# Kernel tuning notes

Hardware: AMD Instinct MI355X
Metric: run time of the kernel (lower is better)

Reference implementation:

```python
import jax, jax.numpy as jnp
import numpy as np

D_MODEL = 512
N_HEADS = 8
B, S = 2, 2048


def setup_inputs() -> dict:
    key = jax.random.key(0)
    ks = jax.random.split(key, 7)
    scale = 1.0 / np.sqrt(D_MODEL)
    return {
        "q": jax.random.normal(ks[0], (B, S, D_MODEL), jnp.float32),
        "k": jax.random.normal(ks[1], (B, S, D_MODEL), jnp.float32),
        "v": jax.random.normal(ks[2], (B, S, D_MODEL), jnp.float32),
        "Wq_w": jax.random.normal(ks[3], (D_MODEL, D_MODEL), jnp.float32) * scale,
        "Wq_b": jnp.zeros((D_MODEL,), jnp.float32),
        "Wc_w": jax.random.normal(ks[4], (D_MODEL, D_MODEL), jnp.float32) * scale,
        "Wc_b": jnp.zeros((D_MODEL,), jnp.float32),
    }


def _split(x, n_heads):
    b, s, d = x.shape
    return x.reshape(b, s, n_heads, d // n_heads).transpose(0, 2, 1, 3)  # [b,h,s,dh]


def reference(q, k, v, Wq_w, Wq_b, Wc_w, Wc_b):
    # NOTE: original code (faithfully) projects q, k, v all with W_q.
    qp = q @ Wq_w.T + Wq_b
    kp = k @ Wq_w.T + Wq_b
    vp = v @ Wq_w.T + Wq_b
    qh = _split(qp, N_HEADS)  # [b,h,s,dh]
    kh = _split(kp, N_HEADS)
    vh = _split(vp, N_HEADS)
    d_tensor = qh.shape[-1]
    scores = jnp.einsum("bhqd,bhkd->bhqk", qh, kh) / jnp.sqrt(jnp.float32(d_tensor))
    att = jax.nn.softmax(scores, axis=-1)
    out = jnp.einsum("bhqk,bhkd->bhqd", att, vh)
    b, h, s, dh = out.shape
    out = out.transpose(0, 2, 1, 3).reshape(b, s, h * dh)
    return out @ Wc_w.T + Wc_b
```

## Files before the change

### kernel.cpp

```cpp
#include <hip/hip_runtime.h>
#include <hip/hip_bf16.h>
#include <stdint.h>


typedef __bf16 bf16;
typedef __bf16 bvec8 __attribute__((ext_vector_type(8)));
typedef __bf16 bvec4 __attribute__((ext_vector_type(4)));
typedef float  fvec4 __attribute__((ext_vector_type(4)));
typedef float  fvec16 __attribute__((ext_vector_type(16)));
typedef int    ivec4 __attribute__((ext_vector_type(4)));

#define MFMA16(a, b, c) __builtin_amdgcn_mfma_f32_16x16x32_bf16(a, b, c, 0, 0, 0)
#define MFMA32(a, b, c) __builtin_amdgcn_mfma_f32_32x32x16_bf16(a, b, c, 0, 0, 0)

__device__ __forceinline__ void async16(const void* g, void* l) {
  __builtin_amdgcn_global_load_lds(
      (__attribute__((address_space(1))) void*)(g),
      (__attribute__((address_space(3))) void*)(l), 16, 0, 0);
}

__global__ void cvt_all(const float* __restrict__ q, const float* __restrict__ k,
                        const float* __restrict__ v, const float* __restrict__ Wq,
                        const float* __restrict__ Wc, bf16* __restrict__ qkvb,
                        bf16* __restrict__ Wq16, bf16* __restrict__ Wc16) {
  const int t = blockIdx.x * 256 + threadIdx.x;
  const float* src;
  bf16* dst;
  size_t i;
  if (t < 786432) {
    const int which = t >> 18;
    i = (size_t)(t & 262143);
    src = (which == 0) ? q : (which == 1) ? k : v;
    dst = qkvb + ((size_t)which << 21);
  } else if (t < 819200) {
    src = Wq; dst = Wq16; i = (size_t)(t - 786432);
  } else {
    src = Wc; dst = Wc16; i = (size_t)(t - 819200);
  }
  fvec4 a = *(const fvec4*)(src + i * 8);
  fvec4 b = *(const fvec4*)(src + i * 8 + 4);
  bvec8 o;
#pragma unroll
  for (int j = 0; j < 4; ++j) { o[j] = (bf16)a[j]; o[j + 4] = (bf16)b[j]; }
  *(bvec8*)(dst + i * 8) = o;
}

__launch_bounds__(256, 3)
__global__ void proj_gemm(const bf16* __restrict__ X, const bf16* __restrict__ W,
                          const float* __restrict__ bias, bf16* __restrict__ Y,
                          bf16* __restrict__ Yt) {
  __shared__ __attribute__((aligned(16))) char As[2][64 * 128];
  __shared__ __attribute__((aligned(16))) char Bs[2][128 * 128];

  const int tid = threadIdx.x;
  const int w = tid >> 6, l = tid & 63;
  const int wr = w >> 1, wc = w & 1;
  const int l15 = l & 15, lg = l >> 4;
  const int bm0 = blockIdx.x * 64;
  const int bn0 = blockIdx.y * 128;

  fvec4 acc[2][4] = {};

  auto stageA = [&](int buf, int k0) {
#pragma unroll
    for (int j = 0; j < 2; ++j) {
      int c = j * 256 + tid;
      int row = c >> 3, g = (c & 7) ^ (row & 7);
      async16(X + (size_t)(bm0 + row) * 512 + k0 + g * 8, &As[buf][c * 16]);
    }
  };
  auto stageB = [&](int buf, int k0) {
#pragma unroll
    for (int j = 0; j < 4; ++j) {
      int c = j * 256 + tid;
      int row = c >> 3, g = (c & 7) ^ (row & 7);
      async16(W + (size_t)(bn0 + row) * 512 + k0 + g * 8, &Bs[buf][c * 16]);
    }
  };

  stageA(0, 0);
  stageB(0, 0);
  __syncthreads();

  for (int t = 0; t < 8; ++t) {
    const int buf = t & 1;
    if (t < 7) { stageA(buf ^ 1, (t + 1) * 64); stageB(buf ^ 1, (t + 1) * 64); }
#pragma unroll
    for (int kk = 0; kk < 2; ++kk) {
      bvec8 af[2], bfr[4];
      const int g = kk * 4 + lg;
#pragma unroll
      for (int m = 0; m < 2; ++m) {
        int r = wr * 32 + m * 16 + l15;
        af[m] = *(const bvec8*)&As[buf][r * 128 + ((g ^ (r & 7)) << 4)];
      }
#pragma unroll
      for (int n = 0; n < 4; ++n) {
        int r = wc * 64 + n * 16 + l15;
        bfr[n] = *(const bvec8*)&Bs[buf][r * 128 + ((g ^ (r & 7)) << 4)];
      }
#pragma unroll
      for (int m = 0; m < 2; ++m)
#pragma unroll
        for (int n = 0; n < 4; ++n) acc[m][n] = MFMA16(af[m], bfr[n], acc[m][n]);
    }
    __syncthreads();
  }

  const bool trans = (bm0 >= 8192);
  const float scl = (bm0 < 4096) ? 0.18033688011112042f : 1.0f;
#pragma unroll
  for (int n = 0; n < 4; ++n) {
    const int col = bn0 + wc * 64 + n * 16 + l15;
    const float bv = bias[col];
#pragma unroll
    for (int m = 0; m < 2; ++m) {
      const int row0 = bm0 + wr * 32 + m * 16 + lg * 4;
      if (!trans) {
#pragma unroll
        for (int r = 0; r < 4; ++r)
          Y[(size_t)(row0 + r) * 512 + col] = (bf16)((acc[m][n][r] + bv) * scl);
      } else {
        const int m0 = row0 - 8192;
        const int b = m0 >> 11, s = m0 & 2047;
        bvec4 v4;
#pragma unroll
        for (int r = 0; r < 4; ++r) v4[r] = (bf16)(acc[m][n][r] + bv);
        *(bvec4*)&Yt[(size_t)(b * 512 + col) * 2048 + s] = v4;
      }
    }
  }
}

__launch_bounds__(256, 4)
__global__ void attn_kernel(const bf16* __restrict__ qp, const bf16* __restrict__ kp,
                            const bf16* __restrict__ vt, bf16* __restrict__ po01,
                            bf16* __restrict__ po23, float* __restrict__ pl) {
  __shared__ __attribute__((aligned(16))) char Ks[2][64 * 128];
  __shared__ __attribute__((aligned(16))) char Vs[2][64 * 128];

  const int tid = threadIdx.x;
  const int w = tid >> 6, l = tid & 63;
  const int l31 = l & 31, hi = l >> 5;
  const int bh = blockIdx.y, b = bh >> 3, h = bh & 7;
  const int half = blockIdx.z;
  const int kvbase = half * 512;
  const int qw0 = blockIdx.x * 128 + w * 32;

  const bf16* kbase = kp + (size_t)(b * 2048) * 512 + h * 64;
  const bf16* vbase = vt + (size_t)(b * 512 + h * 64) * 2048;

  bvec8 qf[4];
  {
    const bf16* qrow = qp + (size_t)(b * 2048 + qw0 + l31) * 512 + h * 64 + hi * 8;
#pragma unroll
    for (int ks = 0; ks < 4; ++ks) qf[ks] = *(const bvec8*)(qrow + ks * 16);
  }
  bvec8 ones;
#pragma unroll
  for (int e = 0; e < 8; ++e) ones[e] = (bf16)1.0f;

  auto stageK = [&](int buf, int kv0) {
#pragma unroll
    for (int j = 0; j < 2; ++j) {
      int c = j * 256 + tid;
      int row = c >> 3, g = (c & 7) ^ (row & 7);
      async16(kbase + (size_t)(kv0 + row) * 512 + g * 8, &Ks[buf][c * 16]);
    }
  };
  auto stageV = [&](int buf, int kv0) {
#pragma unroll
    for (int j = 0; j < 2; ++j) {
      int c = j * 256 + tid;
      int row = c >> 3, g = (c & 7) ^ (row & 7);
      async16(vbase + (size_t)row * 2048 + kv0 + g * 8, &Vs[buf][c * 16]);
    }
  };

  fvec16 oacc[2] = {};
  fvec16 lacc = {};

  stageK(0, kvbase);
  stageV(0, kvbase);
  __syncthreads();

  for (int t = 0; t < 8; ++t) {
    const int buf = t & 1;
    if (t < 7) {
      stageK(buf ^ 1, kvbase + (t + 1) * 64);
      stageV(buf ^ 1, kvbase + (t + 1) * 64);
    }

    fvec16 sac[2] = {};
    __builtin_amdgcn_s_setprio(1);
#pragma unroll
    for (int ks = 0; ks < 4; ++ks) {
      const int chunk = ks * 2 + hi;
#pragma unroll
      for (int kvb = 0; kvb < 2; ++kvb) {
        const int r = kvb * 32 + l31;
        bvec8 kf = *(const bvec8*)&Ks[buf][r * 128 + ((chunk ^ (r & 7)) << 4)];
        sac[kvb] = MFMA32(kf, qf[ks], sac[kvb]);
      }
    }
    __builtin_amdgcn_s_setprio(0);

    ivec4 pw[4];
#pragma unroll
    for (int f = 0; f < 2; ++f) {
      float p[16];
#pragma unroll
      for (int r2 = 0; r2 < 16; ++r2) p[r2] = exp2f(sac[f][r2]);
      int wv[4][2];
#pragma unroll
      for (int m = 0; m < 4; ++m)
#pragma unroll
        for (int i = 0; i < 2; ++i)
          asm("v_cvt_pk_bf16_f32 %0, %1, %2"
              : "=v"(wv[m][i]) : "v"(p[4 * m + 2 * i]), "v"(p[4 * m + 2 * i + 1]));
#pragma unroll
      for (int i = 0; i < 2; ++i) {
        int a0 = wv[0][i], c0 = wv[1][i];
        asm volatile("v_permlane32_swap_b32 %0, %1" : "+v"(a0), "+v"(c0));
        pw[2 * f][i] = a0; pw[2 * f][2 + i] = c0;
        int a1 = wv[2][i], c1 = wv[3][i];
        asm volatile("v_permlane32_swap_b32 %0, %1" : "+v"(a1), "+v"(c1));
        pw[2 * f + 1][i] = a1; pw[2 * f + 1][2 + i] = c1;
      }
    }

    __builtin_amdgcn_s_setprio(1);
#pragma unroll
    for (int ks = 0; ks < 4; ++ks) {
      const bvec8 pb = __builtin_bit_cast(bvec8, pw[ks]);
      const int chunk = ks * 2 + hi;
#pragma unroll
      for (int dhb = 0; dhb < 2; ++dhb) {
        const int r = dhb * 32 + l31;
        bvec8 vf = *(const bvec8*)&Vs[buf][r * 128 + ((chunk ^ (r & 7)) << 4)];
        oacc[dhb] = MFMA32(pb, vf, oacc[dhb]);
      }
      lacc = MFMA32(pb, ones, lacc);
    }
    __builtin_amdgcn_s_setprio(0);
    __syncthreads();
  }

  bf16* pob = ((half < 2) ? po01 : po23) + (size_t)(half & 1) * 2097152;
#pragma unroll
  for (int dhb = 0; dhb < 2; ++dhb)
#pragma unroll
    for (int r2 = 0; r2 < 16; ++r2) {
      const int q = qw0 + (r2 & 3) + 8 * (r2 >> 2) + 4 * hi;
      pob[(size_t)(b * 2048 + q) * 512 + h * 64 + dhb * 32 + l31] =
          (bf16)oacc[dhb][r2];
    }
  if (l31 == 0) {
#pragma unroll
    for (int r2 = 0; r2 < 16; ++r2) {
      const int q = qw0 + (r2 & 3) + 8 * (r2 >> 2) + 4 * hi;
      pl[half * 32768 + (b * 2048 + q) * 8 + h] = lacc[r2];
    }
  }
}

__global__ void combine_kernel(const bf16* __restrict__ po01, const bf16* __restrict__ po23,
                               const float* __restrict__ pl, bf16* __restrict__ att) {
  const int t = blockIdx.x * 256 + threadIdx.x;
  const int row = t >> 6;
  const int c8 = (t & 63) << 3;
  const int h = c8 >> 6;
  const float inv = 1.0f / (pl[row * 8 + h] + pl[32768 + row * 8 + h] +
                            pl[65536 + row * 8 + h] + pl[98304 + row * 8 + h]);
  bvec8 a0 = *(const bvec8*)(po01 + (size_t)row * 512 + c8);
  bvec8 a1 = *(const bvec8*)(po01 + 2097152 + (size_t)row * 512 + c8);
  bvec8 a2 = *(const bvec8*)(po23 + (size_t)row * 512 + c8);
  bvec8 a3 = *(const bvec8*)(po23 + 2097152 + (size_t)row * 512 + c8);
  bvec8 o;
#pragma unroll
  for (int j = 0; j < 8; ++j)
    o[j] = (bf16)((((float)a0[j] + (float)a1[j]) + ((float)a2[j] + (float)a3[j])) * inv);
  *(bvec8*)(att + (size_t)row * 512 + c8) = o;
}

__launch_bounds__(256, 3)
__global__ void out_gemm(const bf16* __restrict__ X, const bf16* __restrict__ W,
                         const float* __restrict__ bias, float* __restrict__ Y) {
  __shared__ __attribute__((aligned(16))) char As[2][64 * 128];
  __shared__ __attribute__((aligned(16))) char Bs[2][128 * 128];

  const int tid = threadIdx.x;
  const int w = tid >> 6, l = tid & 63;
  const int wr = w >> 1, wc = w & 1;
  const int l15 = l & 15, lg = l >> 4;
  const int bm0 = blockIdx.x * 64;
  const int bn0 = blockIdx.y * 128;

  fvec4 acc[2][4] = {};

  auto stageA = [&](int buf, int k0) {
#pragma unroll
    for (int j = 0; j < 2; ++j) {
      int c = j * 256 + tid;
      int row = c >> 3, g = (c & 7) ^ (row & 7);
      async16(X + (size_t)(bm0 + row) * 512 + k0 + g * 8, &As[buf][c * 16]);
    }
  };
  auto stageB = [&](int buf, int k0) {
#pragma unroll
    for (int j = 0; j < 4; ++j) {
      int c = j * 256 + tid;
      int row = c >> 3, g = (c & 7) ^ (row & 7);
      async16(W + (size_t)(bn0 + row) * 512 + k0 + g * 8, &Bs[buf][c * 16]);
    }
  };

  stageA(0, 0);
  stageB(0, 0);
  __syncthreads();

  for (int t = 0; t < 8; ++t) {
    const int buf = t & 1;
    if (t < 7) { stageA(buf ^ 1, (t + 1) * 64); stageB(buf ^ 1, (t + 1) * 64); }
#pragma unroll
    for (int kk = 0; kk < 2; ++kk) {
      bvec8 af[2], bfr[4];
      const int g = kk * 4 + lg;
#pragma unroll
      for (int m = 0; m < 2; ++m) {
        int r = wr * 32 + m * 16 + l15;
        af[m] = *(const bvec8*)&As[buf][r * 128 + ((g ^ (r & 7)) << 4)];
      }
#pragma unroll
      for (int n = 0; n < 4; ++n) {
        int r = wc * 64 + n * 16 + l15;
        bfr[n] = *(const bvec8*)&Bs[buf][r * 128 + ((g ^ (r & 7)) << 4)];
      }
#pragma unroll
      for (int m = 0; m < 2; ++m)
#pragma unroll
        for (int n = 0; n < 4; ++n) acc[m][n] = MFMA16(af[m], bfr[n], acc[m][n]);
    }
    __syncthreads();
  }

#pragma unroll
  for (int n = 0; n < 4; ++n) {
    const int col = bn0 + wc * 64 + n * 16 + l15;
    const float bv = bias[col];
#pragma unroll
    for (int m = 0; m < 2; ++m) {
      const int row0 = bm0 + wr * 32 + m * 16 + lg * 4;
#pragma unroll
      for (int r = 0; r < 4; ++r)
        Y[(size_t)(row0 + r) * 512 + col] = acc[m][n][r] + bv;
    }
  }
}

extern "C" void kernel_launch(void* const* d_in, const int* in_sizes, int n_in,
                              void* d_out, int out_size, void* d_ws, size_t ws_size,
                              hipStream_t stream) {
  const float* q   = (const float*)d_in[0];
  const float* k   = (const float*)d_in[1];
  const float* v   = (const float*)d_in[2];
  const float* Wq  = (const float*)d_in[3];
  const float* Wqb = (const float*)d_in[4];
  const float* Wc  = (const float*)d_in[5];
  const float* Wcb = (const float*)d_in[6];
  float* out = (float*)d_out;

  char* ws = (char*)d_ws;
  const size_t MB = 1u << 20;
  bf16* qkvb = (bf16*)(ws);
  bf16* po01 = (bf16*)(ws);
  bf16* att  = (bf16*)(ws + 8 * MB);
  bf16* Wq16 = (bf16*)(ws + 12 * MB);
  bf16* Wc16 = (bf16*)(ws + 12 * MB + 512 * 1024);
  bf16* qkp  = (bf16*)(ws + 13 * MB);
  bf16* vt   = (bf16*)(ws + 21 * MB);
  bf16* po23 = (bf16*)(ws + 25 * MB);
  float* pl  = (float*)(ws + 33 * MB);

  dim3 bb(256);
  hipLaunchKernelGGL(cvt_all, dim3(3328), bb, 0, stream, q, k, v, Wq, Wc,
                     qkvb, Wq16, Wc16);
  hipLaunchKernelGGL(proj_gemm, dim3(192, 4), bb, 0, stream,
                     qkvb, Wq16, Wqb, qkp, vt);
  hipLaunchKernelGGL(attn_kernel, dim3(16, 16, 4), bb, 0, stream,
                     qkp, qkp + 2097152, vt, po01, po23, pl);
  hipLaunchKernelGGL(combine_kernel, dim3(1024), bb, 0, stream,
                     po01, po23, pl, att);
  hipLaunchKernelGGL(out_gemm, dim3(64, 4), bb, 0, stream,
                     att, Wc16, Wcb, out);
}
```

Before: 71.31 us.

## Fuse split-KV combine into attention via last-block atomic counter

Removes the separate combine kernel. Each attention block increments a per-(bh, q-tile) atomic counter after writing its partial output, and the last of the four KV-split blocks reduces the partials into the final attention output. This drops one kernel launch and its global round trip, at the cost of a memset launch, threadfences, and a serialized tail in the last-arriving blocks. Launch bounds also drop from 4 to 3 waves per SIMD to make room for more registers.

```diff
diff --git a/kernel.cpp b/kernel.cpp
--- a/kernel.cpp
+++ b/kernel.cpp
@@ -132,12 +132,14 @@
   }
 }
 
-__launch_bounds__(256, 4)
+__launch_bounds__(256, 3)
 __global__ void attn_kernel(const bf16* __restrict__ qp, const bf16* __restrict__ kp,
                             const bf16* __restrict__ vt, bf16* __restrict__ po01,
-                            bf16* __restrict__ po23, float* __restrict__ pl) {
+                            bf16* __restrict__ po23, float* __restrict__ pl,
+                            bf16* __restrict__ att, int* __restrict__ cnt) {
   __shared__ __attribute__((aligned(16))) char Ks[2][64 * 128];
   __shared__ __attribute__((aligned(16))) char Vs[2][64 * 128];
+  __shared__ int sOld;
 
   const int tid = threadIdx.x;
   const int w = tid >> 6, l = tid & 63;
@@ -262,25 +264,41 @@
       pl[half * 32768 + (b * 2048 + q) * 8 + h] = lacc[r2];
     }
   }
-}
-
-__global__ void combine_kernel(const bf16* __restrict__ po01, const bf16* __restrict__ po23,
-                               const float* __restrict__ pl, bf16* __restrict__ att) {
-  const int t = blockIdx.x * 256 + threadIdx.x;
-  const int row = t >> 6;
-  const int c8 = (t & 63) << 3;
-  const int h = c8 >> 6;
-  const float inv = 1.0f / (pl[row * 8 + h] + pl[32768 + row * 8 + h] +
-                            pl[65536 + row * 8 + h] + pl[98304 + row * 8 + h]);
-  bvec8 a0 = *(const bvec8*)(po01 + (size_t)row * 512 + c8);
-  bvec8 a1 = *(const bvec8*)(po01 + 2097152 + (size_t)row * 512 + c8);
-  bvec8 a2 = *(const bvec8*)(po23 + (size_t)row * 512 + c8);
-  bvec8 a3 = *(const bvec8*)(po23 + 2097152 + (size_t)row * 512 + c8);
-  bvec8 o;
-#pragma unroll
-  for (int j = 0; j < 8; ++j)
-    o[j] = (bf16)((((float)a0[j] + (float)a1[j]) + ((float)a2[j] + (float)a3[j])) * inv);
-  *(bvec8*)(att + (size_t)row * 512 + c8) = o;
+
+  __threadfence();
+  __syncthreads();
+  if (tid == 0)
+    sOld = __hip_atomic_fetch_add(&cnt[bh * 16 + blockIdx.x], 1,
+                                  __ATOMIC_ACQ_REL, __HIP_MEMORY_SCOPE_AGENT);
+  __syncthreads();
+  if (sOld == 3) {
+    __threadfence();
+    const bf16* pb0 = po01;
+    const bf16* pb1 = po01 + 2097152;
+    const bf16* pb2 = po23;
+    const bf16* pb3 = po23 + 2097152;
+#pragma unroll
+    for (int j = 0; j < 4; ++j) {
+      const int chunk = tid * 4 + j;
+      const int rl = chunk >> 3;
+      const int c8 = (chunk & 7) * 8;
+      const int row = b * 2048 + blockIdx.x * 128 + rl;
+      const int col = h * 64 + c8;
+      const float inv = 1.0f / (pl[row * 8 + h] + pl[32768 + row * 8 + h] +
+                                pl[65536 + row * 8 + h] + pl[98304 + row * 8 + h]);
+      const size_t off = (size_t)row * 512 + col;
+      bvec8 a0 = *(const bvec8*)(pb0 + off);
+      bvec8 a1 = *(const bvec8*)(pb1 + off);
+      bvec8 a2 = *(const bvec8*)(pb2 + off);
+      bvec8 a3 = *(const bvec8*)(pb3 + off);
+      bvec8 o;
+#pragma unroll
+      for (int e = 0; e < 8; ++e)
+        o[e] = (bf16)((((float)a0[e] + (float)a1[e]) +
+                       ((float)a2[e] + (float)a3[e])) * inv);
+      *(bvec8*)(att + off) = o;
+    }
+  }
 }
 
 __launch_bounds__(256, 3)
@@ -381,6 +399,9 @@
   bf16* vt   = (bf16*)(ws + 21 * MB);
   bf16* po23 = (bf16*)(ws + 25 * MB);
   float* pl  = (float*)(ws + 33 * MB);
+  int*   cnt = (int*)(ws + 34 * MB);
+
+  hipMemsetAsync(cnt, 0, 256 * sizeof(int), stream);
 
   dim3 bb(256);
   hipLaunchKernelGGL(cvt_all, dim3(3328), bb, 0, stream, q, k, v, Wq, Wc,
@@ -388,9 +409,7 @@
   hipLaunchKernelGGL(proj_gemm, dim3(192, 4), bb, 0, stream,
                      qkvb, Wq16, Wqb, qkp, vt);
   hipLaunchKernelGGL(attn_kernel, dim3(16, 16, 4), bb, 0, stream,
-                     qkp, qkp + 2097152, vt, po01, po23, pl);
-  hipLaunchKernelGGL(combine_kernel, dim3(1024), bb, 0, stream,
-                     po01, po23, pl, att);
+                     qkp, qkp + 2097152, vt, po01, po23, pl, att, cnt);
   hipLaunchKernelGGL(out_gemm, dim3(64, 4), bb, 0, stream,
                      att, Wc16, Wcb, out);
 }
```

Result: slower. 259.6 us (+264.1%).
